# Kernel tuning notes

Measured on AMD Instinct MI355X. Metric: run time of the kernel, lower is better.

The kernel has to match this reference:

```python
import jax, jax.numpy as jnp
import numpy as np

N_NODES = 100000


def gcn_conv(x, W, b, src, dst, ew, n):
    # PyG GCNConv with add_self_loops=True, symmetric normalization.
    # deg[i] = sum of incoming edge weights at i + 1.0 (self-loop weight 1)
    deg = jax.ops.segment_sum(ew, dst, num_segments=n) + 1.0
    dinv = jax.lax.rsqrt(deg)
    norm = dinv[src] * ew * dinv[dst]          # [E]
    h = x @ W                                  # [N, out]  (lin has no bias)
    msg = h[src] * norm[:, None]               # [E, out] gather + scale
    out = jax.ops.segment_sum(msg, dst, num_segments=n)
    out = out + h * (dinv * dinv)[:, None]     # self-loop contribution
    return out + b


def setup_inputs() -> dict:
    key = jax.random.key(0)
    ks = jax.random.split(key, 12)
    n, f = N_NODES, 128
    e = 1600000

    def lin_init(k, fin, fout):
        s = 1.0 / np.sqrt(fin)
        return jax.random.uniform(k, (fin, fout), jnp.float32, -s, s)

    return {
        "x": jax.random.normal(ks[0], (n, f), jnp.float32),
        "edge_index": jax.random.randint(ks[1], (2, e), 0, n, jnp.int64),
        "edge_attr": jax.random.uniform(ks[2], (e,), jnp.float32),
        "W1": lin_init(ks[3], f, 64),   "b1": jnp.zeros((64,), jnp.float32),
        "W2": lin_init(ks[4], 64, 128), "b2": jnp.zeros((128,), jnp.float32),
        "W3": lin_init(ks[5], 128, 256),"b3": jnp.zeros((256,), jnp.float32),
        "Wl1": lin_init(ks[6], 256, 128),
        "bl1": jax.random.uniform(ks[7], (128,), jnp.float32, -1/16.0, 1/16.0),
        "Wl2": lin_init(ks[8], 128, 10),
        "bl2": jax.random.uniform(ks[9], (10,), jnp.float32, -1/np.sqrt(128), 1/np.sqrt(128)),
    }


def reference(x, edge_index, edge_attr, W1, b1, W2, b2, W3, b3, Wl1, bl1, Wl2, bl2):
    src, dst = edge_index[0], edge_index[1]
    n = x.shape[0]
    h = jax.nn.relu(gcn_conv(x, W1, b1, src, dst, edge_attr, n))
    h = jax.nn.relu(gcn_conv(h, W2, b2, src, dst, edge_attr, n))
    h = jax.nn.relu(gcn_conv(h, W3, b3, src, dst, edge_attr, n))
    g = jnp.max(h, axis=0, keepdims=True)      # global_max_pool, batch=None -> [1, 256]
    g = jax.nn.relu(g @ Wl1 + bl1)
    # dropout p=0.5 is identity in eval mode
    logits = g @ Wl2 + bl2
    return jax.nn.log_softmax(logits, axis=1)
```

## Files before the change

kernel.cpp:

```cpp
#include <hip/hip_runtime.h>
#include <math.h>


typedef unsigned short u16;
typedef unsigned int   u32;
typedef unsigned long long u64;

typedef short bf16x8 __attribute__((ext_vector_type(8)));
typedef float f32x4  __attribute__((ext_vector_type(4)));

#define MAXR 64

__device__ __forceinline__ float bf2f(u16 u) {
    return __uint_as_float(((u32)u) << 16);
}
__device__ __forceinline__ u16 f2bf(float f) {
    u32 u = __float_as_uint(f);
    u32 r = (u + 0x7fffu + ((u >> 16) & 1u)) >> 16;
    return (u16)r;
}
__device__ __forceinline__ u32 pack2(float lo, float hi) {
    return (u32)f2bf(lo) | ((u32)f2bf(hi) << 16);
}


__global__ void deg_rank_kernel(const int* __restrict__ ei, const float* __restrict__ ew,
                                u64* __restrict__ pk, u16* __restrict__ rank, int E) {
    int e = blockIdx.x * blockDim.x + threadIdx.x;
    if (e < E) {
        int d = ei[E + e];
        u64 add = (1ULL << 48) | (u64)((double)ew[e] * 4294967296.0);
        u64 old = atomicAdd(&pk[(size_t)d * 8], add);
        u64 r = old >> 48;
        rank[e] = (u16)(r > 65535 ? 65535 : r);
    }
}

__global__ void scatter_kernel(const int* __restrict__ ei, const float* __restrict__ ew,
                               const u16* __restrict__ rank, uint2* __restrict__ edge2,
                               int n, int E) {
    int e = blockIdx.x * blockDim.x + threadIdx.x;
    if (e < E) {
        int r = (int)rank[e];
        if (r < MAXR) {
            int s = ei[e], d = ei[E + e];
            edge2[(size_t)r * n + d] = make_uint2((u32)s, __float_as_uint(ew[e]));
        }
    }
}

__global__ void finish_deg_kernel(const u64* __restrict__ pk, float* __restrict__ dinv, int n) {
    int i = blockIdx.x * blockDim.x + threadIdx.x;
    if (i < n) {
        double deg = (double)(pk[(size_t)i * 8] & ((1ULL << 48) - 1)) * (1.0 / 4294967296.0);
        dinv[i] = rsqrtf((float)deg + 1.0f);
    }
}

__global__ void cast_scale_kernel(const float* __restrict__ x, const float* __restrict__ dinv,
                                  u16* __restrict__ xs, int n) {
    int idx = blockIdx.x * blockDim.x + threadIdx.x;
    int node = idx >> 4, c = idx & 15;
    if (node < n) {
        float di = dinv[node];
        const float4* p = reinterpret_cast<const float4*>(&x[(size_t)node * 128 + c * 8]);
        float4 a = p[0], b = p[1];
        uint4 o;
        o.x = pack2(di * a.x, di * a.y);
        o.y = pack2(di * a.z, di * a.w);
        o.z = pack2(di * b.x, di * b.y);
        o.w = pack2(di * b.z, di * b.w);
        *reinterpret_cast<uint4*>(&xs[(size_t)node * 128 + c * 8]) = o;
    }
}

template<int FIN, int FOUT>
__global__ void wconv_kernel(const float* __restrict__ W, u16* __restrict__ Wf) {
    int t = blockIdx.x;
    int s = blockIdx.y;
    int l = threadIdx.x;
    int col = t * 16 + (l & 15);
    int k0 = s * 32 + 8 * (l >> 4);
    u32 packed[4];
    for (int jj = 0; jj < 4; ++jj) {
        u16 lo = f2bf(W[(size_t)(k0 + 2 * jj) * FOUT + col]);
        u16 hi = f2bf(W[(size_t)(k0 + 2 * jj + 1) * FOUT + col]);
        packed[jj] = (u32)lo | ((u32)hi << 16);
    }
    u32* dst = (u32*)&Wf[(((size_t)t * (FIN / 32) + s) * 64 + l) * 8];
    dst[0] = packed[0]; dst[1] = packed[1]; dst[2] = packed[2]; dst[3] = packed[3];
}

template<int FIN, int FOUT, bool FUSE_MAX, bool SCALE_OUT>
__global__ __launch_bounds__(256)
void fused_layer_kernel(const u16* __restrict__ R, const u64* __restrict__ pk,
                        const uint2* __restrict__ edge2, const float* __restrict__ dinv,
                        const u16* __restrict__ Wf, const float* __restrict__ b,
                        u16* __restrict__ Rout, float* __restrict__ g, int n) {
    constexpr int KS  = FIN / 32;
    constexpr int NT  = FOUT / 16;
    constexpr int TPN = FIN / 8;
    constexpr int NPB = 256 / TPN;
    constexpr int NIT = 64 / NPB;
    __shared__ u16 Asw[4][KS][64][8];
    __shared__ int gsm[256];
    int tid = threadIdx.x;
    int gbase = blockIdx.x * 64;

    if (FUSE_MAX) gsm[tid] = 0;

    int sub = tid / TPN;
    int q   = tid % TPN;
    #pragma unroll
    for (int it = 0; it < NIT; ++it) {
        int m = it * NPB + sub;
        int node = gbase + m;
        float acc[8];
        #pragma unroll
        for (int j = 0; j < 8; ++j) acc[j] = 0.f;

        if (node < n) {
            int cnt = (int)(pk[(size_t)node * 8] >> 48);
            if (cnt > MAXR) cnt = MAXR;
            float di = dinv[node];

            auto fmadd = [&](float w, uint4 h) {
                acc[0] += w * bf2f((u16)h.x);  acc[1] += w * bf2f((u16)(h.x >> 16));
                acc[2] += w * bf2f((u16)h.y);  acc[3] += w * bf2f((u16)(h.y >> 16));
                acc[4] += w * bf2f((u16)h.z);  acc[5] += w * bf2f((u16)(h.z >> 16));
                acc[6] += w * bf2f((u16)h.w);  acc[7] += w * bf2f((u16)(h.w >> 16));
            };

            uint4 sv = *reinterpret_cast<const uint4*>(&R[(size_t)node * FIN + q * 8]);
            fmadd(1.0f, sv);

            const uint2* ecol = edge2 + node;
            int e = 0;
            for (; e + 4 <= cnt; e += 4) {
                uint2 ed0 = ecol[(size_t)e * n];
                uint2 ed1 = ecol[(size_t)(e + 1) * n];
                uint2 ed2 = ecol[(size_t)(e + 2) * n];
                uint2 ed3 = ecol[(size_t)(e + 3) * n];
                uint4 h0 = *reinterpret_cast<const uint4*>(&R[(size_t)ed0.x * FIN + q * 8]);
                uint4 h1 = *reinterpret_cast<const uint4*>(&R[(size_t)ed1.x * FIN + q * 8]);
                uint4 h2 = *reinterpret_cast<const uint4*>(&R[(size_t)ed2.x * FIN + q * 8]);
                uint4 h3 = *reinterpret_cast<const uint4*>(&R[(size_t)ed3.x * FIN + q * 8]);
                fmadd(__uint_as_float(ed0.y), h0);
                fmadd(__uint_as_float(ed1.y), h1);
                fmadd(__uint_as_float(ed2.y), h2);
                fmadd(__uint_as_float(ed3.y), h3);
            }
            for (; e < cnt; ++e) {
                uint2 ed = ecol[(size_t)e * n];
                uint4 hv = *reinterpret_cast<const uint4*>(&R[(size_t)ed.x * FIN + q * 8]);
                fmadd(__uint_as_float(ed.y), hv);
            }

            #pragma unroll
            for (int j = 0; j < 8; ++j) acc[j] *= di;
        }

        uint4 o;
        o.x = pack2(acc[0], acc[1]);
        o.y = pack2(acc[2], acc[3]);
        o.z = pack2(acc[4], acc[5]);
        o.w = pack2(acc[6], acc[7]);
        *reinterpret_cast<uint4*>(&Asw[m >> 4][q >> 2][((q & 3) << 4) | (m & 15)][0]) = o;
    }
    __syncthreads();

    int w = tid >> 6, lane = tid & 63;
    int nodeq = gbase + w * 16 + ((lane >> 4) << 2);

    bf16x8 a[KS];
    #pragma unroll
    for (int s = 0; s < KS; ++s)
        a[s] = *reinterpret_cast<const bf16x8*>(&Asw[w][s][lane][0]);

    float dv[4];
    if (SCALE_OUT) {
        #pragma unroll
        for (int r = 0; r < 4; ++r) {
            int node = nodeq + r;
            dv[r] = (node < n) ? dinv[node] : 0.f;
        }
    }

    int col0 = lane & 15;
    #pragma unroll
    for (int t = 0; t < NT; ++t) {
        f32x4 acc = {0.f, 0.f, 0.f, 0.f};
        #pragma unroll
        for (int s = 0; s < KS; ++s) {
            bf16x8 bf = *reinterpret_cast<const bf16x8*>(&Wf[(((size_t)t * KS + s) * 64 + lane) * 8]);
            acc = __builtin_amdgcn_mfma_f32_16x16x32_bf16(a[s], bf, acc, 0, 0, 0);
        }
        int col = t * 16 + col0;
        float bb = b[col];
        if (FUSE_MAX) {
            float ml = 0.0f;
            #pragma unroll
            for (int r = 0; r < 4; ++r) {
                int node = nodeq + r;
                float v = acc[r] + bb;
                if (node < n) ml = fmaxf(ml, v);
            }
            ml = fmaxf(ml, __shfl_xor(ml, 16));
            ml = fmaxf(ml, __shfl_xor(ml, 32));
            if ((lane >> 4) == 0) atomicMax(&gsm[col], __float_as_int(ml));
        } else {
            #pragma unroll
            for (int r = 0; r < 4; ++r) {
                int node = nodeq + r;
                if (node < n) {
                    float v = fmaxf(acc[r] + bb, 0.0f);
                    if (SCALE_OUT) v *= dv[r];
                    Rout[(size_t)node * FOUT + col] = f2bf(v);
                }
            }
        }
    }
    if (FUSE_MAX) {
        __syncthreads();
        atomicMax(&((int*)g)[tid], gsm[tid]);
    }
}


__global__ void head_kernel(const float* __restrict__ g, const float* __restrict__ Wl1,
                            const float* __restrict__ bl1, const float* __restrict__ Wl2,
                            const float* __restrict__ bl2, float* __restrict__ out) {
    __shared__ float gs[256];
    __shared__ float ys[128];
    __shared__ float ls[10];
    int t = threadIdx.x;
    gs[t] = g[t];
    __syncthreads();
    if (t < 128) {
        float acc = bl1[t];
        for (int k = 0; k < 256; ++k) acc += gs[k] * Wl1[k * 128 + t];
        ys[t] = fmaxf(acc, 0.0f);
    }
    __syncthreads();
    if (t < 10) {
        float acc = bl2[t];
        for (int j = 0; j < 128; ++j) acc += ys[j] * Wl2[j * 10 + t];
        ls[t] = acc;
    }
    __syncthreads();
    if (t == 0) {
        float m = ls[0];
        for (int c = 1; c < 10; ++c) m = fmaxf(m, ls[c]);
        float se = 0.0f;
        for (int c = 0; c < 10; ++c) se += expf(ls[c] - m);
        float lse = logf(se);
        for (int c = 0; c < 10; ++c) out[c] = ls[c] - m - lse;
    }
}


static inline int cdiv(int a, int b) { return (a + b - 1) / b; }

extern "C" void kernel_launch(void* const* d_in, const int* in_sizes, int n_in,
                              void* d_out, int out_size, void* d_ws, size_t ws_size,
                              hipStream_t stream) {
    const float* x   = (const float*)d_in[0];
    const int*   ei  = (const int*)d_in[1];
    const float* ew  = (const float*)d_in[2];
    const float* W1  = (const float*)d_in[3];
    const float* b1  = (const float*)d_in[4];
    const float* W2  = (const float*)d_in[5];
    const float* b2  = (const float*)d_in[6];
    const float* W3  = (const float*)d_in[7];
    const float* b3  = (const float*)d_in[8];
    const float* Wl1 = (const float*)d_in[9];
    const float* bl1 = (const float*)d_in[10];
    const float* Wl2 = (const float*)d_in[11];
    const float* bl2 = (const float*)d_in[12];

    const int n = in_sizes[0] / 128;
    const int E = in_sizes[1] / 2;

    char* p = (char*)d_ws;
    auto alloc = [&](size_t bytes) { char* q = p; p += (bytes + 255) & ~(size_t)255; return q; };
    u64*   pk    = (u64*)  alloc((size_t)n * 64);
    float* dinv  = (float*)alloc((size_t)n * 4);
    u16*   rank  = (u16*)  alloc((size_t)E * 2);
    uint2* edge2 = (uint2*)alloc((size_t)MAXR * n * 8);
    u16*   xs    = (u16*)  alloc((size_t)n * 128 * 2);
    u16*   r2    = (u16*)  alloc((size_t)n * 64 * 2);
    u16*   r3    = (u16*)  alloc((size_t)n * 128 * 2);
    u16*   W1f   = (u16*)  alloc((size_t)128 * 64 * 2);
    u16*   W2f   = (u16*)  alloc((size_t)64 * 128 * 2);
    u16*   W3f   = (u16*)  alloc((size_t)128 * 256 * 2);
    float* g     = (float*)alloc(256 * 4);

    hipMemsetAsync(pk, 0, (size_t)n * 64, stream);
    hipMemsetAsync(g,  0, 256 * 4, stream);

    int eb = cdiv(E, 256);
    deg_rank_kernel<<<eb, 256, 0, stream>>>(ei, ew, pk, rank, E);
    scatter_kernel<<<eb, 256, 0, stream>>>(ei, ew, rank, edge2, n, E);
    finish_deg_kernel<<<cdiv(n, 256), 256, 0, stream>>>(pk, dinv, n);
    cast_scale_kernel<<<cdiv(n * 16, 256), 256, 0, stream>>>(x, dinv, xs, n);

    wconv_kernel<128, 64><<<dim3(64 / 16, 128 / 32), 64, 0, stream>>>(W1, W1f);
    wconv_kernel<64, 128><<<dim3(128 / 16, 64 / 32), 64, 0, stream>>>(W2, W2f);
    wconv_kernel<128, 256><<<dim3(256 / 16, 128 / 32), 64, 0, stream>>>(W3, W3f);

    fused_layer_kernel<128, 64, false, true><<<cdiv(n, 64), 256, 0, stream>>>(xs, pk, edge2, dinv, W1f, b1, r2, nullptr, n);
    fused_layer_kernel<64, 128, false, true><<<cdiv(n, 64), 256, 0, stream>>>(r2, pk, edge2, dinv, W2f, b2, r3, nullptr, n);
    fused_layer_kernel<128, 256, true, false><<<cdiv(n, 64), 256, 0, stream>>>(r3, pk, edge2, dinv, W3f, b3, nullptr, g, n);

    head_kernel<<<1, 256, 0, stream>>>(g, Wl1, bl1, Wl2, bl2, (float*)d_out);
}
```

Baseline: 347.1 us.

## Reorder layer 1 as transform-then-aggregate over 64-wide features

```diff
diff --git a/kernel.cpp b/kernel.cpp
--- a/kernel.cpp
+++ b/kernel.cpp
@@ -54,23 +54,6 @@
     if (i < n) {
         double deg = (double)(pk[(size_t)i * 8] & ((1ULL << 48) - 1)) * (1.0 / 4294967296.0);
         dinv[i] = rsqrtf((float)deg + 1.0f);
-    }
-}
-
-__global__ void cast_scale_kernel(const float* __restrict__ x, const float* __restrict__ dinv,
-                                  u16* __restrict__ xs, int n) {
-    int idx = blockIdx.x * blockDim.x + threadIdx.x;
-    int node = idx >> 4, c = idx & 15;
-    if (node < n) {
-        float di = dinv[node];
-        const float4* p = reinterpret_cast<const float4*>(&x[(size_t)node * 128 + c * 8]);
-        float4 a = p[0], b = p[1];
-        uint4 o;
-        o.x = pack2(di * a.x, di * a.y);
-        o.y = pack2(di * a.z, di * a.w);
-        o.z = pack2(di * b.x, di * b.y);
-        o.w = pack2(di * b.z, di * b.w);
-        *reinterpret_cast<uint4*>(&xs[(size_t)node * 128 + c * 8]) = o;
     }
 }
 
@@ -89,6 +72,126 @@
     }
     u32* dst = (u32*)&Wf[(((size_t)t * (FIN / 32) + s) * 64 + l) * 8];
     dst[0] = packed[0]; dst[1] = packed[1]; dst[2] = packed[2]; dst[3] = packed[3];
+}
+
+template<int FIN, int FOUT>
+__global__ __launch_bounds__(256)
+void gemm0_kernel(const float* __restrict__ x, const float* __restrict__ dinv,
+                  const u16* __restrict__ Wf, u16* __restrict__ Y, int n) {
+    constexpr int KS = FIN / 32;
+    constexpr int NT = FOUT / 16;
+    constexpr int Q8 = FIN / 8;
+    __shared__ u16 Asw[4][KS][64][8];
+    int tid = threadIdx.x;
+    int gbase = blockIdx.x * 64;
+
+    for (int idx = tid; idx < 64 * Q8; idx += 256) {
+        int m = idx / Q8, q = idx - m * Q8;
+        int gn = gbase + m;
+        uint4 o = make_uint4(0, 0, 0, 0);
+        if (gn < n) {
+            float di = dinv[gn];
+            const float4* p = reinterpret_cast<const float4*>(&x[(size_t)gn * FIN + q * 8]);
+            float4 a = p[0], b = p[1];
+            o.x = pack2(di * a.x, di * a.y);
+            o.y = pack2(di * a.z, di * a.w);
+            o.z = pack2(di * b.x, di * b.y);
+            o.w = pack2(di * b.z, di * b.w);
+        }
+        *reinterpret_cast<uint4*>(&Asw[m >> 4][q >> 2][((q & 3) << 4) | (m & 15)][0]) = o;
+    }
+    __syncthreads();
+
+    int w = tid >> 6, lane = tid & 63;
+    int nodeq = gbase + w * 16 + ((lane >> 4) << 2);
+
+    bf16x8 a[KS];
+    #pragma unroll
+    for (int s = 0; s < KS; ++s)
+        a[s] = *reinterpret_cast<const bf16x8*>(&Asw[w][s][lane][0]);
+
+    int col0 = lane & 15;
+    #pragma unroll
+    for (int t = 0; t < NT; ++t) {
+        f32x4 acc = {0.f, 0.f, 0.f, 0.f};
+        #pragma unroll
+        for (int s = 0; s < KS; ++s) {
+            bf16x8 bf = *reinterpret_cast<const bf16x8*>(&Wf[(((size_t)t * KS + s) * 64 + lane) * 8]);
+            acc = __builtin_amdgcn_mfma_f32_16x16x32_bf16(a[s], bf, acc, 0, 0, 0);
+        }
+        int col = t * 16 + col0;
+        #pragma unroll
+        for (int r = 0; r < 4; ++r) {
+            int node = nodeq + r;
+            if (node < n) Y[(size_t)node * FOUT + col] = f2bf(acc[r]);
+        }
+    }
+}
+
+template<int F>
+__global__ __launch_bounds__(256)
+void agg_epi_kernel(const u16* __restrict__ Y, const u64* __restrict__ pk,
+                    const uint2* __restrict__ edge2, const float* __restrict__ dinv,
+                    const float* __restrict__ b, u16* __restrict__ Rout, int n) {
+    constexpr int TPN = F / 8;
+    constexpr int NPB = 256 / TPN;
+    int t = threadIdx.x;
+    int node = blockIdx.x * NPB + t / TPN;
+    if (node >= n) return;
+    int j8 = (t % TPN) * 8;
+    int cnt = (int)(pk[(size_t)node * 8] >> 48);
+    if (cnt > MAXR) cnt = MAXR;
+    float di = dinv[node];
+
+    uint4 sv = *reinterpret_cast<const uint4*>(&Y[(size_t)node * F + j8]);
+    float acc0, acc1, acc2, acc3, acc4, acc5, acc6, acc7;
+    acc0 = bf2f((u16)sv.x);  acc1 = bf2f((u16)(sv.x >> 16));
+    acc2 = bf2f((u16)sv.y);  acc3 = bf2f((u16)(sv.y >> 16));
+    acc4 = bf2f((u16)sv.z);  acc5 = bf2f((u16)(sv.z >> 16));
+    acc6 = bf2f((u16)sv.w);  acc7 = bf2f((u16)(sv.w >> 16));
+
+    const uint2* ecol = edge2 + node;
+    int e = 0;
+    for (; e + 4 <= cnt; e += 4) {
+        uint2 ed0 = ecol[(size_t)e * n];
+        uint2 ed1 = ecol[(size_t)(e + 1) * n];
+        uint2 ed2 = ecol[(size_t)(e + 2) * n];
+        uint2 ed3 = ecol[(size_t)(e + 3) * n];
+        uint4 h0 = *reinterpret_cast<const uint4*>(&Y[(size_t)ed0.x * F + j8]);
+        uint4 h1 = *reinterpret_cast<const uint4*>(&Y[(size_t)ed1.x * F + j8]);
+        uint4 h2 = *reinterpret_cast<const uint4*>(&Y[(size_t)ed2.x * F + j8]);
+        uint4 h3 = *reinterpret_cast<const uint4*>(&Y[(size_t)ed3.x * F + j8]);
+        float w0 = __uint_as_float(ed0.y);
+        float w1 = __uint_as_float(ed1.y);
+        float w2 = __uint_as_float(ed2.y);
+        float w3 = __uint_as_float(ed3.y);
+        acc0 += w0 * bf2f((u16)h0.x) + w1 * bf2f((u16)h1.x) + w2 * bf2f((u16)h2.x) + w3 * bf2f((u16)h3.x);
+        acc1 += w0 * bf2f((u16)(h0.x >> 16)) + w1 * bf2f((u16)(h1.x >> 16)) + w2 * bf2f((u16)(h2.x >> 16)) + w3 * bf2f((u16)(h3.x >> 16));
+        acc2 += w0 * bf2f((u16)h0.y) + w1 * bf2f((u16)h1.y) + w2 * bf2f((u16)h2.y) + w3 * bf2f((u16)h3.y);
+        acc3 += w0 * bf2f((u16)(h0.y >> 16)) + w1 * bf2f((u16)(h1.y >> 16)) + w2 * bf2f((u16)(h2.y >> 16)) + w3 * bf2f((u16)(h3.y >> 16));
+        acc4 += w0 * bf2f((u16)h0.z) + w1 * bf2f((u16)h1.z) + w2 * bf2f((u16)h2.z) + w3 * bf2f((u16)h3.z);
+        acc5 += w0 * bf2f((u16)(h0.z >> 16)) + w1 * bf2f((u16)(h1.z >> 16)) + w2 * bf2f((u16)(h2.z >> 16)) + w3 * bf2f((u16)(h3.z >> 16));
+        acc6 += w0 * bf2f((u16)h0.w) + w1 * bf2f((u16)h1.w) + w2 * bf2f((u16)h2.w) + w3 * bf2f((u16)h3.w);
+        acc7 += w0 * bf2f((u16)(h0.w >> 16)) + w1 * bf2f((u16)(h1.w >> 16)) + w2 * bf2f((u16)(h2.w >> 16)) + w3 * bf2f((u16)(h3.w >> 16));
+    }
+    for (; e < cnt; ++e) {
+        uint2 ed = ecol[(size_t)e * n];
+        float w = __uint_as_float(ed.y);
+        uint4 hv = *reinterpret_cast<const uint4*>(&Y[(size_t)ed.x * F + j8]);
+        acc0 += w * bf2f((u16)hv.x);  acc1 += w * bf2f((u16)(hv.x >> 16));
+        acc2 += w * bf2f((u16)hv.y);  acc3 += w * bf2f((u16)(hv.y >> 16));
+        acc4 += w * bf2f((u16)hv.z);  acc5 += w * bf2f((u16)(hv.z >> 16));
+        acc6 += w * bf2f((u16)hv.w);  acc7 += w * bf2f((u16)(hv.w >> 16));
+    }
+
+    const float4* bp = reinterpret_cast<const float4*>(&b[j8]);
+    float4 b0 = bp[0], b1v = bp[1];
+    uint4 o;
+    o.x = pack2(di * fmaxf(di * acc0 + b0.x, 0.f), di * fmaxf(di * acc1 + b0.y, 0.f));
+    o.y = pack2(di * fmaxf(di * acc2 + b0.z, 0.f), di * fmaxf(di * acc3 + b0.w, 0.f));
+    o.z = pack2(di * fmaxf(di * acc4 + b1v.x, 0.f), di * fmaxf(di * acc5 + b1v.y, 0.f));
+    o.w = pack2(di * fmaxf(di * acc6 + b1v.z, 0.f), di * fmaxf(di * acc7 + b1v.w, 0.f));
+    *reinterpret_cast<uint4*>(&Rout[(size_t)node * F + j8]) = o;
 }
 
 template<int FIN, int FOUT, bool FUSE_MAX, bool SCALE_OUT>
@@ -287,7 +390,7 @@
     float* dinv  = (float*)alloc((size_t)n * 4);
     u16*   rank  = (u16*)  alloc((size_t)E * 2);
     uint2* edge2 = (uint2*)alloc((size_t)MAXR * n * 8);
-    u16*   xs    = (u16*)  alloc((size_t)n * 128 * 2);
+    u16*   y1    = (u16*)  alloc((size_t)n * 64 * 2);
     u16*   r2    = (u16*)  alloc((size_t)n * 64 * 2);
     u16*   r3    = (u16*)  alloc((size_t)n * 128 * 2);
     u16*   W1f   = (u16*)  alloc((size_t)128 * 64 * 2);
@@ -302,13 +405,13 @@
     deg_rank_kernel<<<eb, 256, 0, stream>>>(ei, ew, pk, rank, E);
     scatter_kernel<<<eb, 256, 0, stream>>>(ei, ew, rank, edge2, n, E);
     finish_deg_kernel<<<cdiv(n, 256), 256, 0, stream>>>(pk, dinv, n);
-    cast_scale_kernel<<<cdiv(n * 16, 256), 256, 0, stream>>>(x, dinv, xs, n);
 
     wconv_kernel<128, 64><<<dim3(64 / 16, 128 / 32), 64, 0, stream>>>(W1, W1f);
     wconv_kernel<64, 128><<<dim3(128 / 16, 64 / 32), 64, 0, stream>>>(W2, W2f);
     wconv_kernel<128, 256><<<dim3(256 / 16, 128 / 32), 64, 0, stream>>>(W3, W3f);
 
-    fused_layer_kernel<128, 64, false, true><<<cdiv(n, 64), 256, 0, stream>>>(xs, pk, edge2, dinv, W1f, b1, r2, nullptr, n);
+    gemm0_kernel<128, 64><<<cdiv(n, 64), 256, 0, stream>>>(x, dinv, W1f, y1, n);
+    agg_epi_kernel<64><<<cdiv(n, 32), 256, 0, stream>>>(y1, pk, edge2, dinv, b1, r2, n);
     fused_layer_kernel<64, 128, false, true><<<cdiv(n, 64), 256, 0, stream>>>(r2, pk, edge2, dinv, W2f, b2, r3, nullptr, n);
     fused_layer_kernel<128, 256, true, false><<<cdiv(n, 64), 256, 0, stream>>>(r3, pk, edge2, dinv, W3f, b3, nullptr, g, n);
 
```

Result: faster. 311.3 us (-10.3%).
